# Kernel tuning notes

Hardware: AMD Instinct MI355X
Metric: run time of the kernel (lower is better)

Reference implementation:

```python
import jax, jax.numpy as jnp
import numpy as np

B, T, D = 1, 2048, 1024
H = 16
HD = D // H
K = 4
FF = 4 * D
LAYERS = 24
EPS = 1.1920929e-07  # torch.finfo(float32).eps, RMSNorm default


def setup_inputs() -> dict:
    key = jax.random.key(0)
    ks = jax.random.split(key, 16)
    s = 0.02
    return {
        "x": jax.random.normal(ks[0], (B, T, D), jnp.float32),
        "gamma": jax.random.uniform(ks[1], (D,), jnp.float32),
        "beta": jax.random.normal(ks[2], (D,), jnp.float32) * 0.1,
        "iter_scale": jax.random.uniform(ks[3], (1,), jnp.float32),
        "qkv_bases": jax.random.normal(ks[4], (K, 3 * D, D), jnp.float32) * s,
        "o_bases": jax.random.normal(ks[5], (K, D, D), jnp.float32) * s,
        "gate_bases": jax.random.normal(ks[6], (K, FF, D), jnp.float32) * s,
        "up_bases": jax.random.normal(ks[7], (K, FF, D), jnp.float32) * s,
        "down_bases": jax.random.normal(ks[8], (K, D, FF), jnp.float32) * s,
        "alpha_qkv": jax.random.normal(ks[9], (LAYERS, K), jnp.float32) * 0.1 + jnp.eye(LAYERS, K)[:, :K] * 0.0 + jnp.concatenate([jnp.ones((LAYERS, 1)), jnp.zeros((LAYERS, K - 1))], axis=1),
        "alpha_o": jnp.concatenate([jnp.ones((LAYERS, 1)), jnp.zeros((LAYERS, K - 1))], axis=1) + jax.random.normal(ks[10], (LAYERS, K)) * 0.1,
        "alpha_gate": jnp.concatenate([jnp.ones((LAYERS, 1)), jnp.zeros((LAYERS, K - 1))], axis=1) + jax.random.normal(ks[11], (LAYERS, K)) * 0.1,
        "alpha_up": jnp.concatenate([jnp.ones((LAYERS, 1)), jnp.zeros((LAYERS, K - 1))], axis=1) + jax.random.normal(ks[12], (LAYERS, K)) * 0.1,
        "alpha_down": jnp.concatenate([jnp.ones((LAYERS, 1)), jnp.zeros((LAYERS, K - 1))], axis=1) + jax.random.normal(ks[13], (LAYERS, K)) * 0.1,
        "norm1_w": jnp.ones((D,), jnp.float32),
        "norm2_w": jnp.ones((D,), jnp.float32),
        "layer_idx": 5,
    }


def _rmsnorm(x, w):
    return x * jax.lax.rsqrt(jnp.mean(x * x, axis=-1, keepdims=True) + EPS) * w


def reference(x, gamma, beta, iter_scale, qkv_bases, o_bases, gate_bases, up_bases,
              down_bases, alpha_qkv, alpha_o, alpha_gate, alpha_up, alpha_down,
              norm1_w, norm2_w, layer_idx):
    Bx, Tx, Dx = x.shape
    # --- attention sub-block ---
    h = _rmsnorm(x, norm1_w) * gamma + beta
    W_qkv = jnp.einsum('k,kij->ij', alpha_qkv[layer_idx], qkv_bases)  # [3D, D]
    qkv = jnp.einsum('btd,od->bto', h, W_qkv).reshape(Bx, Tx, 3, H, HD)
    qkv = jnp.transpose(qkv, (2, 0, 3, 1, 4))  # [3, B, H, T, HD]
    q, k, v = qkv[0], qkv[1], qkv[2]
    scores = jnp.einsum('bhqd,bhkd->bhqk', q, k) / jnp.sqrt(jnp.asarray(HD, x.dtype))
    causal = jnp.tril(jnp.ones((Tx, Tx), bool))
    scores = jnp.where(causal, scores, jnp.asarray(-jnp.inf, scores.dtype))
    attn = jax.nn.softmax(scores, axis=-1)
    out = jnp.einsum('bhqk,bhkd->bhqd', attn, v)
    out = jnp.transpose(out, (0, 2, 1, 3)).reshape(Bx, Tx, Dx)
    W_o = jnp.einsum('k,kij->ij', alpha_o[layer_idx], o_bases)
    x_attn = x + jnp.einsum('btd,od->bto', out, W_o)
    # --- SwiGLU FFN sub-block ---
    h2 = _rmsnorm(x_attn, norm2_w) * gamma + beta
    W_g = jnp.einsum('k,kij->ij', alpha_gate[layer_idx], gate_bases)
    W_u = jnp.einsum('k,kij->ij', alpha_up[layer_idx], up_bases)
    W_d = jnp.einsum('k,kij->ij', alpha_down[layer_idx], down_bases)
    gate = jnp.einsum('btd,fd->btf', h2, W_g)
    up = jnp.einsum('btd,fd->btf', h2, W_u)
    ffn_out = jnp.einsum('btf,df->btd', jax.nn.silu(gate) * up, W_d)
    block_out = x_attn + ffn_out
    return x + (block_out - x) * iter_scale
```

## Files before the change

kernel.cpp:

```cpp
#include <hip/hip_runtime.h>
#include <hip/hip_bf16.h>
#include <math.h>

typedef __bf16 bf16;
typedef __bf16 bf16x8 __attribute__((ext_vector_type(8)));
typedef __bf16 bf16x4 __attribute__((ext_vector_type(4)));
typedef float f32x4 __attribute__((ext_vector_type(4)));

#define EPSc 1.1920929e-07f
#define LOG2E 1.44269504f

static __device__ __forceinline__ void glds16(const void* g, void* l) {
  __builtin_amdgcn_global_load_lds((const __attribute__((address_space(1))) void*)g,
                                   (__attribute__((address_space(3))) void*)l, 16, 0, 0);
}

static __device__ __forceinline__ bf16x4 comb4(const float* b0, const float* b1,
                                               const float* b2, const float* b3,
                                               float a0, float a1, float a2, float a3) {
  float4 v0 = *(const float4*)b0, v1 = *(const float4*)b1;
  float4 v2 = *(const float4*)b2, v3 = *(const float4*)b3;
  bf16x4 o;
  o[0] = (bf16)(a0*v0.x + a1*v1.x + a2*v2.x + a3*v3.x);
  o[1] = (bf16)(a0*v0.y + a1*v1.y + a2*v2.y + a3*v3.y);
  o[2] = (bf16)(a0*v0.z + a1*v1.z + a2*v2.z + a3*v3.z);
  o[3] = (bf16)(a0*v0.w + a1*v1.w + a2*v2.w + a3*v3.w);
  return o;
}

__global__ __launch_bounds__(256)
void prep1(const float* __restrict__ qkv_b, const float* __restrict__ a_qkv,
           const float* __restrict__ o_b,   const float* __restrict__ a_o,
           const float* __restrict__ x, const float* __restrict__ n1w,
           const float* __restrict__ gamma, const float* __restrict__ beta,
           const int* __restrict__ lidx,
           bf16* __restrict__ Wqkv, bf16* __restrict__ Wo, bf16* __restrict__ hbuf) {
  const int bid = blockIdx.x, tid = threadIdx.x;
  if (bid < 4096) {
    int li = lidx[0];
    const float* base; const float* al; bf16* out; size_t flat, n;
    if (bid < 3072) { base = qkv_b; al = a_qkv; out = Wqkv; flat = (size_t)bid << 10; n = (size_t)3072*1024; }
    else            { base = o_b;   al = a_o;   out = Wo;   flat = (size_t)(bid-3072) << 10; n = (size_t)1024*1024; }
    float a0 = al[li*4], a1 = al[li*4+1], a2 = al[li*4+2], a3 = al[li*4+3];
    size_t off = flat + tid*4;
    bf16x4 o = comb4(base+off, base+n+off, base+2*n+off, base+3*n+off, a0, a1, a2, a3);
    *(bf16x4*)&out[off] = o;
  } else {
    int row = bid - 4096, t = tid;
    const float4* xr = (const float4*)(x + (size_t)row*1024);
    float4 v = xr[t];
    float ss = v.x*v.x + v.y*v.y + v.z*v.z + v.w*v.w;
    #pragma unroll
    for (int off = 32; off > 0; off >>= 1) ss += __shfl_down(ss, off, 64);
    __shared__ float red[4];
    if ((t & 63) == 0) red[t >> 6] = ss;
    __syncthreads();
    float tot = red[0] + red[1] + red[2] + red[3];
    float r = rsqrtf(tot * (1.0f/1024.0f) + EPSc);
    float4 wv = ((const float4*)n1w)[t];
    float4 gv = ((const float4*)gamma)[t];
    float4 bv = ((const float4*)beta)[t];
    bf16x4 o;
    o[0] = (bf16)(v.x*r*wv.x*gv.x + bv.x);
    o[1] = (bf16)(v.y*r*wv.y*gv.y + bv.y);
    o[2] = (bf16)(v.z*r*wv.z*gv.z + bv.z);
    o[3] = (bf16)(v.w*r*wv.w*gv.w + bv.w);
    *(bf16x4*)&hbuf[(size_t)row*1024 + t*4] = o;
  }
}

__global__ __launch_bounds__(256) void rmsnorm_k(const float* __restrict__ x,
                                                 const float* __restrict__ w,
                                                 const float* __restrict__ gamma,
                                                 const float* __restrict__ beta,
                                                 bf16* __restrict__ out) {
  int row = blockIdx.x, t = threadIdx.x;
  const float4* xr = (const float4*)(x + (size_t)row*1024);
  float4 v = xr[t];
  float ss = v.x*v.x + v.y*v.y + v.z*v.z + v.w*v.w;
  #pragma unroll
  for (int off = 32; off > 0; off >>= 1) ss += __shfl_down(ss, off, 64);
  __shared__ float red[4];
  if ((t & 63) == 0) red[t >> 6] = ss;
  __syncthreads();
  float tot = red[0] + red[1] + red[2] + red[3];
  float r = rsqrtf(tot * (1.0f/1024.0f) + EPSc);
  float4 wv = ((const float4*)w)[t];
  float4 gv = ((const float4*)gamma)[t];
  float4 bv = ((const float4*)beta)[t];
  bf16x4 o;
  o[0] = (bf16)(v.x*r*wv.x*gv.x + bv.x);
  o[1] = (bf16)(v.y*r*wv.y*gv.y + bv.y);
  o[2] = (bf16)(v.z*r*wv.z*gv.z + bv.z);
  o[3] = (bf16)(v.w*r*wv.w*gv.w + bv.w);
  *(bf16x4*)&out[(size_t)row*1024 + t*4] = o;
}

template<int EP, int NTW>
__global__ __launch_bounds__(256)
void gemm_bt(const bf16* __restrict__ A, const bf16* __restrict__ Bw,
             int M, int N, int K, int lda, int ldb, int gx,
             float* __restrict__ outf, bf16* __restrict__ outb,
             const float* __restrict__ auxf, const float* __restrict__ auxf2,
             const float* __restrict__ iscale) {
  constexpr int BN = NTW * 32;
  __shared__ __align__(16) bf16 As[2][128*64];
  __shared__ __align__(16) bf16 Bs[2][BN*64];
  const int nwg = gridDim.x;
  const int orig = blockIdx.x;
  const int wg = (orig & 7) * (nwg >> 3) + (orig >> 3);
  const int tn0 = (wg % gx) * BN, tm0 = (wg / gx) * 128;
  const int tid = threadIdx.x, wave = tid >> 6, lane = tid & 63;
  const int lr = lane & 15, lg = lane >> 4;
  const int wr = wave >> 1, wc = wave & 1;
  f32x4 acc[4][NTW] = {};
  const int rs = lane >> 3;
  const int sc = (((lane & 7) ^ rs) << 3);
  const int x0 = ((lg ^ (lr & 7)) << 3);
  const int x1 = (((4 + lg) ^ (lr & 7)) << 3);

  const bf16* Abase = A + (size_t)tm0 * lda;
  const bf16* Bbase = Bw + (size_t)tn0 * ldb;

  auto stage = [&](bf16* as, bf16* bs, int k0) {
    #pragma unroll
    for (int j = 0; j < 4; ++j) {
      int chunk = wave*4 + j;
      int r = chunk*8 + rs;
      glds16(Abase + (size_t)r*lda + k0 + sc, as + chunk*512 + lane*8);
    }
    #pragma unroll
    for (int j = 0; j < NTW; ++j) {
      int chunk = wave*NTW + j;
      int r = chunk*8 + rs;
      glds16(Bbase + (size_t)r*ldb + k0 + sc, bs + chunk*512 + lane*8);
    }
  };
  auto comp = [&](const bf16* as, const bf16* bs) {
    #pragma unroll
    for (int kk = 0; kk < 2; ++kk) {
      const int x = kk ? x1 : x0;
      bf16x8 av[4], bv[NTW];
      #pragma unroll
      for (int m = 0; m < 4; ++m) av[m] = *(const bf16x8*)&as[(wr*64 + m*16 + lr)*64 + x];
      #pragma unroll
      for (int n = 0; n < NTW; ++n) bv[n] = *(const bf16x8*)&bs[(wc*NTW*16 + n*16 + lr)*64 + x];
      #pragma unroll
      for (int m = 0; m < 4; ++m)
        #pragma unroll
        for (int n = 0; n < NTW; ++n)
          acc[m][n] = __builtin_amdgcn_mfma_f32_16x16x32_bf16(av[m], bv[n], acc[m][n], 0, 0, 0);
    }
  };

  bf16 *a0 = As[0], *a1 = As[1], *b0 = Bs[0], *b1 = Bs[1];
  stage(a0, b0, 0);
  __syncthreads();
  for (int k0 = 64; k0 < K; k0 += 64) {
    stage(a1, b1, k0);
    comp(a0, b0);
    __syncthreads();
    bf16* t;
    t = a0; a0 = a1; a1 = t;
    t = b0; b0 = b1; b1 = t;
  }
  comp(a0, b0);

  float its = 0.f;
  if constexpr (EP == 4) its = iscale[0];
  #pragma unroll
  for (int m = 0; m < 4; ++m)
    #pragma unroll
    for (int n = 0; n < NTW; ++n)
      #pragma unroll
      for (int i = 0; i < 4; ++i) {
        int row = tm0 + wr*64 + m*16 + lg*4 + i;
        int col = tn0 + wc*NTW*16 + n*16 + lr;
        size_t idx = (size_t)row * N + col;
        float v = acc[m][n][i];
        if constexpr (EP == 0) outb[idx] = (bf16)v;
        else if constexpr (EP == 1) outf[idx] = auxf[idx] + v;
        else if constexpr (EP == 4) {
          float xv = auxf[idx], xa = auxf2[idx];
          outf[idx] = xv + (xa + v - xv) * its;
        }
      }
}

__global__ __launch_bounds__(512, 2)
void gemm_gu256(const bf16* __restrict__ A, const bf16* __restrict__ Bw,
                bf16* __restrict__ outb) {
  __shared__ __align__(16) bf16 L[2][2][2][8192];
  const int orig = blockIdx.x;
  const int wg = (orig & 7) * 32 + (orig >> 3);
  const int tn0 = (wg & 31) * 256, tm0 = (wg >> 5) * 256;
  const int tid = threadIdx.x, wave = tid >> 6, lane = tid & 63;
  const int lr = lane & 15, lg = lane >> 4;
  const int wr = wave >> 2, wn = wave & 3;
  const int rs8 = lane >> 3;
  const int gc8 = (((lane & 7) ^ rs8) << 3);
  const int xk0 = ((lg ^ (lr & 7)) << 3);
  const int xk1 = (((4 + lg) ^ (lr & 7)) << 3);
  f32x4 acc[8][4] = {};

  const bf16* Ab = A + (size_t)tm0 * 1024;
  const bf16* Bb = Bw + (size_t)tn0 * 1024;

  auto stage_half = [&](bf16* dst, const bf16* gbase, int half, int k0) {
    #pragma unroll
    for (int l = 0; l < 2; ++l) {
      int r = half*128 + (wave*2 + l)*8 + rs8;
      glds16(gbase + (size_t)r*1024 + k0 + gc8, dst + (wave*2 + l)*512 + lane*8);
    }
  };

  stage_half(&L[0][0][0][0], Ab, 0, 0);
  stage_half(&L[0][0][1][0], Ab, 1, 0);
  stage_half(&L[0][1][0][0], Bb, 0, 0);
  stage_half(&L[0][1][1][0], Bb, 1, 0);
  stage_half(&L[1][1][0][0], Bb, 0, 64);
  stage_half(&L[1][1][1][0], Bb, 1, 64);
  asm volatile("s_waitcnt vmcnt(4)" ::: "memory");
  __builtin_amdgcn_s_barrier();

  for (int t = 0; t < 16; ++t) {
    const int b = t & 1;
    const bf16* ah = &L[b][0][wr][0];
    const bf16* bh = &L[b][1][wn >> 1][0];
    bf16x8 breg[4][2];
    #pragma unroll
    for (int p = 0; p < 4; ++p) {
      if (p == 0) {
        #pragma unroll
        for (int n = 0; n < 4; ++n) {
          int row = (wn & 1)*64 + n*16 + lr;
          breg[n][0] = *(const bf16x8*)&bh[row*64 + xk0];
          breg[n][1] = *(const bf16x8*)&bh[row*64 + xk1];
        }
      }
      bf16x8 av[2][2];
      #pragma unroll
      for (int mi = 0; mi < 2; ++mi) {
        int row = p*32 + mi*16 + lr;
        av[mi][0] = *(const bf16x8*)&ah[row*64 + xk0];
        av[mi][1] = *(const bf16x8*)&ah[row*64 + xk1];
      }
      if (p == 0 && t < 15) stage_half(&L[b^1][0][0][0], Ab, 0, (t+1)*64);
      if (p == 1 && t < 15) stage_half(&L[b^1][0][1][0], Ab, 1, (t+1)*64);
      if (p == 2 && t < 14) stage_half(&L[b][1][0][0], Bb, 0, (t+2)*64);
      if (p == 3 && t < 14) stage_half(&L[b][1][1][0], Bb, 1, (t+2)*64);
      __builtin_amdgcn_s_barrier();
      __builtin_amdgcn_s_setprio(1);
      #pragma unroll
      for (int mi = 0; mi < 2; ++mi)
        #pragma unroll
        for (int n = 0; n < 4; ++n) {
          acc[p*2+mi][n] = __builtin_amdgcn_mfma_f32_16x16x32_bf16(av[mi][0], breg[n][0], acc[p*2+mi][n], 0, 0, 0);
          acc[p*2+mi][n] = __builtin_amdgcn_mfma_f32_16x16x32_bf16(av[mi][1], breg[n][1], acc[p*2+mi][n], 0, 0, 0);
        }
      __builtin_amdgcn_s_setprio(0);
      if (p == 3) {
        if (t >= 14) asm volatile("s_waitcnt vmcnt(0)" ::: "memory");
        else         asm volatile("s_waitcnt vmcnt(4)" ::: "memory");
      }
      __builtin_amdgcn_s_barrier();
    }
  }

  #pragma unroll
  for (int mf = 0; mf < 8; ++mf)
    #pragma unroll
    for (int j = 0; j < 2; ++j)
      #pragma unroll
      for (int i = 0; i < 4; ++i) {
        int row = tm0 + wr*128 + mf*16 + lg*4 + i;
        int col = (tn0 >> 1) + wn*32 + j*16 + lr;
        float g = acc[mf][2*j][i], u = acc[mf][2*j+1][i];
        float s = g / (1.f + __builtin_amdgcn_exp2f(-g * LOG2E));
        outb[(size_t)row * 4096 + col] = (bf16)(s * u);
      }
}

__global__ __launch_bounds__(256)
void attn_mega(const bf16* __restrict__ qkv, bf16* __restrict__ out,
               const float* __restrict__ gate_b, const float* __restrict__ up_b,
               const float* __restrict__ down_b,
               const float* __restrict__ a_gate, const float* __restrict__ a_up,
               const float* __restrict__ a_down, const int* __restrict__ lidx,
               bf16* __restrict__ Wgu, bf16* __restrict__ Wd) {
  __shared__ __align__(16) bf16 Ks[2][64*72];
  __shared__ __align__(16) bf16 Vt[2][64*66];
  __shared__ __align__(16) bf16 Ps[4][16*68];
  const int bid = blockIdx.x;
  const int tid = threadIdx.x;

  if (bid < 256) {
    const int cb = bid;
    int li = lidx[0];
    float g0 = a_gate[li*4], g1 = a_gate[li*4+1], g2 = a_gate[li*4+2], g3 = a_gate[li*4+3];
    float u0 = a_up[li*4],   u1 = a_up[li*4+1],   u2 = a_up[li*4+2],   u3 = a_up[li*4+3];
    float d0 = a_down[li*4], d1 = a_down[li*4+1], d2 = a_down[li*4+2], d3 = a_down[li*4+3];
    const size_t PS = (size_t)4096 * 1024;
    for (int it = 0; it < 48; ++it) {
      int chunk = it * 256 + cb;
      if (chunk < 8192) {
        int r = chunk, w = r & 31;
        int f = ((r >> 5) << 4) + (w & 15);
        const float* base = (w < 16) ? gate_b : up_b;
        float a0 = (w < 16) ? g0 : u0, a1 = (w < 16) ? g1 : u1;
        float a2 = (w < 16) ? g2 : u2, a3 = (w < 16) ? g3 : u3;
        size_t src = (size_t)f*1024 + tid*4;
        bf16x4 o = comb4(base+src, base+PS+src, base+2*PS+src, base+3*PS+src, a0, a1, a2, a3);
        *(bf16x4*)&Wgu[((size_t)r << 10) + tid*4] = o;
      } else {
        size_t off = ((size_t)(chunk - 8192) << 10) + tid*4;
        bf16x4 o = comb4(down_b+off, down_b+PS+off, down_b+2*PS+off, down_b+3*PS+off, d0, d1, d2, d3);
        *(bf16x4*)&Wd[off] = o;
      }
    }
    return;
  }

  const int a = bid - 256;
  const int qb = 31 - (a >> 4);
  const int h = (a & 7) + 8 * ((a >> 3) & 1);
  const int wave = tid >> 6, lane = tid & 63;
  const int lr = lane & 15, lg = lane >> 4;
  const int q0 = qb * 64;

  bf16x8 qf[2];
  {
    const bf16* qrow = qkv + (size_t)(q0 + wave*16 + lr)*3072 + h*64;
    qf[0] = *(const bf16x8*)(qrow + lg*8);
    qf[1] = *(const bf16x8*)(qrow + 32 + lg*8);
  }
  f32x4 o[4] = {};
  float mrow = -__builtin_inff(), lrow = 0.f;
  const int xsrc = (lane & 48) + ((lane >> 4) << 2);

  const int r0 = tid >> 3, r1 = (tid + 256) >> 3;
  const int c0 = (tid & 7) << 3;
  const bf16* kb = qkv + 1024 + h*64 + c0;
  const bf16* vb = qkv + 2048 + h*64 + c0;

  bf16x8 kreg[2], vreg[2];
  auto stage_load = [&](int kv0) {
    kreg[0] = *(const bf16x8*)(kb + (size_t)(kv0 + r0)*3072);
    kreg[1] = *(const bf16x8*)(kb + (size_t)(kv0 + r1)*3072);
    vreg[0] = *(const bf16x8*)(vb + (size_t)(kv0 + r0)*3072);
    vreg[1] = *(const bf16x8*)(vb + (size_t)(kv0 + r1)*3072);
  };
  auto stage_write = [&](int buf) {
    *(bf16x8*)&Ks[buf][r0*72 + c0] = kreg[0];
    *(bf16x8*)&Ks[buf][r1*72 + c0] = kreg[1];
    #pragma unroll
    for (int e = 0; e < 8; ++e) Vt[buf][(c0 + e)*66 + r0] = vreg[0][e];
    #pragma unroll
    for (int e = 0; e < 8; ++e) Vt[buf][(c0 + e)*66 + r1] = vreg[1][e];
  };

  stage_load(0);
  stage_write(0);
  __syncthreads();
  int cur = 0;

  const float C = 0.125f * LOG2E;

  for (int t = 0; t <= qb; ++t) {
    const int kv0 = t * 64;
    if (t < qb) stage_load(kv0 + 64);

    f32x4 s[4] = {};
    __builtin_amdgcn_s_setprio(1);
    #pragma unroll
    for (int n = 0; n < 4; ++n) {
      bf16x8 k0f = *(const bf16x8*)&Ks[cur][(n*16 + lr)*72 + lg*8];
      s[n] = __builtin_amdgcn_mfma_f32_16x16x32_bf16(k0f, qf[0], s[n], 0, 0, 0);
      bf16x8 k1f = *(const bf16x8*)&Ks[cur][(n*16 + lr)*72 + 32 + lg*8];
      s[n] = __builtin_amdgcn_mfma_f32_16x16x32_bf16(k1f, qf[1], s[n], 0, 0, 0);
    }
    __builtin_amdgcn_s_setprio(0);

    if (t == qb) {
      const int qv = q0 + wave*16 + lr;
      #pragma unroll
      for (int n = 0; n < 4; ++n)
        #pragma unroll
        for (int i = 0; i < 4; ++i)
          if (kv0 + n*16 + lg*4 + i > qv) s[n][i] = -__builtin_inff();
    }

    float mnew;
    {
      f32x4 t0 = s[0], t1 = s[1];
      #pragma unroll
      for (int i = 0; i < 4; ++i) { t0[i] = fmaxf(t0[i], s[2][i]); t1[i] = fmaxf(t1[i], s[3][i]); }
      float a0 = fmaxf(t0[0], t0[1]), a1 = fmaxf(t0[2], t0[3]);
      float b0 = fmaxf(t1[0], t1[1]), b1 = fmaxf(t1[2], t1[3]);
      mnew = fmaxf(fmaxf(a0, a1), fmaxf(b0, b1));
    }
    mnew = fmaxf(mnew, __shfl_xor(mnew, 16, 64));
    mnew = fmaxf(mnew, __shfl_xor(mnew, 32, 64));

    float pmn = mnew * C;
    if (__any(pmn > mrow + 8.f)) {
      float mt = fmaxf(mrow, pmn);
      float fc = __builtin_amdgcn_exp2f(mrow - mt);
      mrow = mt;
      lrow *= fc;
      #pragma unroll
      for (int i = 0; i < 4; ++i) {
        float fci = __shfl(fc, xsrc + i, 64);
        #pragma unroll
        for (int nd = 0; nd < 4; ++nd) o[nd][i] *= fci;
      }
    }

    float rsum = 0.f;
    #pragma unroll
    for (int n = 0; n < 4; ++n)
      #pragma unroll
      for (int i = 0; i < 4; ++i) {
        float e = __builtin_amdgcn_exp2f(__builtin_fmaf(s[n][i], C, -mrow));
        s[n][i] = e;
        rsum += e;
      }
    rsum += __shfl_xor(rsum, 16, 64);
    rsum += __shfl_xor(rsum, 32, 64);
    lrow += rsum;

    #pragma unroll
    for (int n = 0; n < 4; ++n) {
      bf16x4 p4;
      #pragma unroll
      for (int i = 0; i < 4; ++i) p4[i] = (bf16)s[n][i];
      *(bf16x4*)&Ps[wave][lr*68 + n*16 + lg*4] = p4;
    }
    asm volatile("s_waitcnt lgkmcnt(0)" ::: "memory");
    __builtin_amdgcn_s_setprio(1);
    #pragma unroll
    for (int kk = 0; kk < 2; ++kk) {
      bf16x8 pf = *(const bf16x8*)&Ps[wave][lr*68 + kk*32 + lg*8];
      #pragma unroll
      for (int nd = 0; nd < 4; ++nd) {
        bf16x8 vf = *(const bf16x8*)&Vt[cur][(nd*16 + lr)*66 + kk*32 + lg*8];
        o[nd] = __builtin_amdgcn_mfma_f32_16x16x32_bf16(pf, vf, o[nd], 0, 0, 0);
      }
    }
    __builtin_amdgcn_s_setprio(0);
    if (t < qb) {
      stage_write(cur ^ 1);
      __syncthreads();
      cur ^= 1;
    }
  }
  #pragma unroll
  for (int i = 0; i < 4; ++i) {
    float li = __shfl(lrow, xsrc + i, 64);
    float inv = 1.f / li;
    #pragma unroll
    for (int nd = 0; nd < 4; ++nd)
      out[(size_t)(q0 + wave*16 + lg*4 + i)*1024 + h*64 + nd*16 + lr] = (bf16)(o[nd][i]*inv);
  }
}

extern "C" void kernel_launch(void* const* d_in, const int* in_sizes, int n_in,
                              void* d_out, int out_size, void* d_ws, size_t ws_size,
                              hipStream_t stream) {
  const float* x        = (const float*)d_in[0];
  const float* gamma    = (const float*)d_in[1];
  const float* beta     = (const float*)d_in[2];
  const float* iscale   = (const float*)d_in[3];
  const float* qkv_b    = (const float*)d_in[4];
  const float* o_b      = (const float*)d_in[5];
  const float* gate_b   = (const float*)d_in[6];
  const float* up_b     = (const float*)d_in[7];
  const float* down_b   = (const float*)d_in[8];
  const float* a_qkv    = (const float*)d_in[9];
  const float* a_o      = (const float*)d_in[10];
  const float* a_gate   = (const float*)d_in[11];
  const float* a_up     = (const float*)d_in[12];
  const float* a_down   = (const float*)d_in[13];
  const float* n1w      = (const float*)d_in[14];
  const float* n2w      = (const float*)d_in[15];
  const int*   lidx     = (const int*)d_in[16];

  char* p = (char*)d_ws;
  auto alloc = [&](size_t bytes) { char* r = p; p += (bytes + 255) & ~(size_t)255; return r; };
  bf16*  Wqkv = (bf16*)alloc((size_t)3072*1024*2);
  bf16*  Wo   = (bf16*)alloc((size_t)1024*1024*2);
  bf16*  Wgu  = (bf16*)alloc((size_t)8192*1024*2);
  bf16*  Wd   = (bf16*)alloc((size_t)1024*4096*2);
  bf16*  hbuf = (bf16*)alloc((size_t)2048*1024*2);
  bf16*  qkvb = (bf16*)alloc((size_t)2048*3072*2);
  bf16*  attn = (bf16*)alloc((size_t)2048*1024*2);
  float* xat  = (float*)alloc((size_t)2048*1024*4);
  bf16*  h2   = (bf16*)alloc((size_t)2048*1024*2);
  bf16*  act  = (bf16*)alloc((size_t)2048*4096*2);
  float* out  = (float*)d_out;

  prep1<<<6144, 256, 0, stream>>>(qkv_b, a_qkv, o_b, a_o, x, n1w, gamma, beta, lidx,
                                  Wqkv, Wo, hbuf);
  gemm_bt<0,4><<<24*16, 256, 0, stream>>>(hbuf, Wqkv, 2048, 3072, 1024, 1024, 1024, 24,
                                          nullptr, qkvb, nullptr, nullptr, nullptr);
  attn_mega<<<768, 256, 0, stream>>>(qkvb, attn, gate_b, up_b, down_b,
                                     a_gate, a_up, a_down, lidx, Wgu, Wd);
  gemm_bt<1,2><<<16*16, 256, 0, stream>>>(attn, Wo, 2048, 1024, 1024, 1024, 1024, 16,
                                          xat, nullptr, x, nullptr, nullptr);
  rmsnorm_k<<<2048, 256, 0, stream>>>(xat, n2w, gamma, beta, h2);
  gemm_gu256<<<256, 512, 0, stream>>>(h2, Wgu, act);
  gemm_bt<4,2><<<16*16, 256, 0, stream>>>(act, Wd, 2048, 1024, 4096, 4096, 4096, 16,
                                          out, nullptr, x, xat, iscale);
}
```

Measured before the change: 193.5 us.

## Enlarge attention query tile to 128 rows with two 16-row tiles per wave

Each attention block now handles 128 query rows (32 per wave, two 16-row sub-tiles) instead of 64, so every K/V tile staged into LDS feeds twice as many MFMAs. This halves the attention block count and the K/V global loads and LDS staging per query, and reuses each K and V fragment across both sub-tiles. In exchange, register pressure rises, there are fewer blocks and the causal workload is coarser, which may hurt load balance. The mask condition is generalised to the per-wave diagonal, and the max reference is clamped to guard against fully masked rows.

```diff
diff --git a/kernel.cpp b/kernel.cpp
--- a/kernel.cpp
+++ b/kernel.cpp
@@ -290,7 +290,7 @@
                bf16* __restrict__ Wgu, bf16* __restrict__ Wd) {
   __shared__ __align__(16) bf16 Ks[2][64*72];
   __shared__ __align__(16) bf16 Vt[2][64*66];
-  __shared__ __align__(16) bf16 Ps[4][16*68];
+  __shared__ __align__(16) bf16 Ps[4][2][16*72];
   const int bid = blockIdx.x;
   const int tid = threadIdx.x;
 
@@ -322,23 +322,27 @@
   }
 
   const int a = bid - 256;
-  const int qb = 31 - (a >> 4);
-  const int h = (a & 7) + 8 * ((a >> 3) & 1);
+  const int qb = 15 - (a >> 4);
+  const int h = a & 15;
   const int wave = tid >> 6, lane = tid & 63;
   const int lr = lane & 15, lg = lane >> 4;
-  const int q0 = qb * 64;
-
-  bf16x8 qf[2];
-  {
-    const bf16* qrow = qkv + (size_t)(q0 + wave*16 + lr)*3072 + h*64;
-    qf[0] = *(const bf16x8*)(qrow + lg*8);
-    qf[1] = *(const bf16x8*)(qrow + 32 + lg*8);
+  const int q0 = qb * 128;
+  const int qw = q0 + wave * 32;
+
+  bf16x8 qf[2][2];
+  #pragma unroll
+  for (int qt = 0; qt < 2; ++qt) {
+    const bf16* qrow = qkv + (size_t)(qw + qt*16 + lr)*3072 + h*64;
+    qf[qt][0] = *(const bf16x8*)(qrow + lg*8);
+    qf[qt][1] = *(const bf16x8*)(qrow + 32 + lg*8);
   }
-  f32x4 o[4] = {};
-  float mrow = -__builtin_inff(), lrow = 0.f;
-  const int xsrc = (lane & 48) + ((lane >> 4) << 2);
-
-  const int r0 = tid >> 3, r1 = (tid + 256) >> 3;
+  f32x4 o[2][4] = {};
+  float mrow[2], lrow[2];
+  mrow[0] = mrow[1] = -__builtin_inff();
+  lrow[0] = lrow[1] = 0.f;
+  const int xsrc = (lane & 48) | (lg << 2);
+
+  const int r0 = tid >> 3, r1 = r0 + 32;
   const int c0 = (tid & 7) << 3;
   const bf16* kb = qkv + 1024 + h*64 + c0;
   const bf16* vb = qkv + 2048 + h*64 + c0;
@@ -365,103 +369,117 @@
   int cur = 0;
 
   const float C = 0.125f * LOG2E;
-
-  for (int t = 0; t <= qb; ++t) {
+  const int nt = 2 * (qb + 1);
+
+  for (int t = 0; t < nt; ++t) {
     const int kv0 = t * 64;
-    if (t < qb) stage_load(kv0 + 64);
-
-    f32x4 s[4] = {};
+    if (t < nt-1) stage_load(kv0 + 64);
+
+    f32x4 s[2][4] = {};
     __builtin_amdgcn_s_setprio(1);
     #pragma unroll
     for (int n = 0; n < 4; ++n) {
       bf16x8 k0f = *(const bf16x8*)&Ks[cur][(n*16 + lr)*72 + lg*8];
-      s[n] = __builtin_amdgcn_mfma_f32_16x16x32_bf16(k0f, qf[0], s[n], 0, 0, 0);
       bf16x8 k1f = *(const bf16x8*)&Ks[cur][(n*16 + lr)*72 + 32 + lg*8];
-      s[n] = __builtin_amdgcn_mfma_f32_16x16x32_bf16(k1f, qf[1], s[n], 0, 0, 0);
+      #pragma unroll
+      for (int qt = 0; qt < 2; ++qt) {
+        s[qt][n] = __builtin_amdgcn_mfma_f32_16x16x32_bf16(k0f, qf[qt][0], s[qt][n], 0, 0, 0);
+        s[qt][n] = __builtin_amdgcn_mfma_f32_16x16x32_bf16(k1f, qf[qt][1], s[qt][n], 0, 0, 0);
+      }
     }
     __builtin_amdgcn_s_setprio(0);
 
-    if (t == qb) {
-      const int qv = q0 + wave*16 + lr;
-      #pragma unroll
-      for (int n = 0; n < 4; ++n)
+    if (kv0 + 63 > qw) {
+      #pragma unroll
+      for (int qt = 0; qt < 2; ++qt) {
+        const int qv = qw + qt*16 + lr;
         #pragma unroll
-        for (int i = 0; i < 4; ++i)
-          if (kv0 + n*16 + lg*4 + i > qv) s[n][i] = -__builtin_inff();
-    }
-
-    float mnew;
-    {
-      f32x4 t0 = s[0], t1 = s[1];
-      #pragma unroll
-      for (int i = 0; i < 4; ++i) { t0[i] = fmaxf(t0[i], s[2][i]); t1[i] = fmaxf(t1[i], s[3][i]); }
+        for (int n = 0; n < 4; ++n)
+          #pragma unroll
+          for (int i = 0; i < 4; ++i)
+            if (kv0 + n*16 + lg*4 + i > qv) s[qt][n][i] = -__builtin_inff();
+      }
+    }
+
+    float pmn[2];
+    #pragma unroll
+    for (int qt = 0; qt < 2; ++qt) {
+      f32x4 t0 = s[qt][0], t1 = s[qt][1];
+      #pragma unroll
+      for (int i = 0; i < 4; ++i) { t0[i] = fmaxf(t0[i], s[qt][2][i]); t1[i] = fmaxf(t1[i], s[qt][3][i]); }
       float a0 = fmaxf(t0[0], t0[1]), a1 = fmaxf(t0[2], t0[3]);
       float b0 = fmaxf(t1[0], t1[1]), b1 = fmaxf(t1[2], t1[3]);
-      mnew = fmaxf(fmaxf(a0, a1), fmaxf(b0, b1));
-    }
-    mnew = fmaxf(mnew, __shfl_xor(mnew, 16, 64));
-    mnew = fmaxf(mnew, __shfl_xor(mnew, 32, 64));
-
-    float pmn = mnew * C;
-    if (__any(pmn > mrow + 8.f)) {
-      float mt = fmaxf(mrow, pmn);
-      float fc = __builtin_amdgcn_exp2f(mrow - mt);
-      mrow = mt;
-      lrow *= fc;
-      #pragma unroll
-      for (int i = 0; i < 4; ++i) {
-        float fci = __shfl(fc, xsrc + i, 64);
+      float mnew = fmaxf(fmaxf(a0, a1), fmaxf(b0, b1));
+      mnew = fmaxf(mnew, __shfl_xor(mnew, 16, 64));
+      mnew = fmaxf(mnew, __shfl_xor(mnew, 32, 64));
+      pmn[qt] = mnew * C;
+    }
+    bool grow = (pmn[0] > mrow[0] + 8.f) || (pmn[1] > mrow[1] + 8.f);
+    if (__any(grow)) {
+      #pragma unroll
+      for (int qt = 0; qt < 2; ++qt) {
+        float mt = fmaxf(mrow[qt], pmn[qt]);
+        float fc = __builtin_amdgcn_exp2f(mrow[qt] - mt);
+        mrow[qt] = mt;
+        lrow[qt] *= fc;
         #pragma unroll
-        for (int nd = 0; nd < 4; ++nd) o[nd][i] *= fci;
-      }
-    }
-
-    float rsum = 0.f;
-    #pragma unroll
-    for (int n = 0; n < 4; ++n)
-      #pragma unroll
-      for (int i = 0; i < 4; ++i) {
-        float e = __builtin_amdgcn_exp2f(__builtin_fmaf(s[n][i], C, -mrow));
-        s[n][i] = e;
-        rsum += e;
-      }
-    rsum += __shfl_xor(rsum, 16, 64);
-    rsum += __shfl_xor(rsum, 32, 64);
-    lrow += rsum;
-
-    #pragma unroll
-    for (int n = 0; n < 4; ++n) {
-      bf16x4 p4;
-      #pragma unroll
-      for (int i = 0; i < 4; ++i) p4[i] = (bf16)s[n][i];
-      *(bf16x4*)&Ps[wave][lr*68 + n*16 + lg*4] = p4;
+        for (int i = 0; i < 4; ++i) {
+          float fci = __shfl(fc, xsrc + i, 64);
+          #pragma unroll
+          for (int nd = 0; nd < 4; ++nd) o[qt][nd][i] *= fci;
+        }
+      }
+    }
+    #pragma unroll
+    for (int qt = 0; qt < 2; ++qt) {
+      float mref = fmaxf(mrow[qt], -3e38f);
+      float rsum = 0.f;
+      #pragma unroll
+      for (int n = 0; n < 4; ++n) {
+        bf16x4 p4;
+        #pragma unroll
+        for (int i = 0; i < 4; ++i) {
+          float e = __builtin_amdgcn_exp2f(__builtin_fmaf(s[qt][n][i], C, -mref));
+          rsum += e;
+          p4[i] = (bf16)e;
+        }
+        *(bf16x4*)&Ps[wave][qt][lr*72 + n*16 + lg*4] = p4;
+      }
+      rsum += __shfl_xor(rsum, 16, 64);
+      rsum += __shfl_xor(rsum, 32, 64);
+      lrow[qt] += rsum;
     }
     asm volatile("s_waitcnt lgkmcnt(0)" ::: "memory");
-    __builtin_amdgcn_s_setprio(1);
+
     #pragma unroll
     for (int kk = 0; kk < 2; ++kk) {
-      bf16x8 pf = *(const bf16x8*)&Ps[wave][lr*68 + kk*32 + lg*8];
+      bf16x8 pf0 = *(const bf16x8*)&Ps[wave][0][lr*72 + kk*32 + lg*8];
+      bf16x8 pf1 = *(const bf16x8*)&Ps[wave][1][lr*72 + kk*32 + lg*8];
+      __builtin_amdgcn_s_setprio(1);
       #pragma unroll
       for (int nd = 0; nd < 4; ++nd) {
         bf16x8 vf = *(const bf16x8*)&Vt[cur][(nd*16 + lr)*66 + kk*32 + lg*8];
-        o[nd] = __builtin_amdgcn_mfma_f32_16x16x32_bf16(pf, vf, o[nd], 0, 0, 0);
-      }
-    }
-    __builtin_amdgcn_s_setprio(0);
-    if (t < qb) {
+        o[0][nd] = __builtin_amdgcn_mfma_f32_16x16x32_bf16(pf0, vf, o[0][nd], 0, 0, 0);
+        o[1][nd] = __builtin_amdgcn_mfma_f32_16x16x32_bf16(pf1, vf, o[1][nd], 0, 0, 0);
+      }
+      __builtin_amdgcn_s_setprio(0);
+    }
+    if (t < nt-1) {
       stage_write(cur ^ 1);
       __syncthreads();
       cur ^= 1;
     }
   }
   #pragma unroll
-  for (int i = 0; i < 4; ++i) {
-    float li = __shfl(lrow, xsrc + i, 64);
-    float inv = 1.f / li;
-    #pragma unroll
-    for (int nd = 0; nd < 4; ++nd)
-      out[(size_t)(q0 + wave*16 + lg*4 + i)*1024 + h*64 + nd*16 + lr] = (bf16)(o[nd][i]*inv);
-  }
+  for (int qt = 0; qt < 2; ++qt)
+    #pragma unroll
+    for (int i = 0; i < 4; ++i) {
+      float li = __shfl(lrow[qt], xsrc + i, 64);
+      float inv = 1.f / li;
+      #pragma unroll
+      for (int nd = 0; nd < 4; ++nd)
+        out[(size_t)(qw + qt*16 + lg*4 + i)*1024 + h*64 + nd*16 + lr] = (bf16)(o[qt][nd][i]*inv);
+    }
 }
 
 extern "C" void kernel_launch(void* const* d_in, const int* in_sizes, int n_in,
@@ -503,7 +521,7 @@
                                   Wqkv, Wo, hbuf);
   gemm_bt<0,4><<<24*16, 256, 0, stream>>>(hbuf, Wqkv, 2048, 3072, 1024, 1024, 1024, 24,
                                           nullptr, qkvb, nullptr, nullptr, nullptr);
-  attn_mega<<<768, 256, 0, stream>>>(qkvb, attn, gate_b, up_b, down_b,
+  attn_mega<<<512, 256, 0, stream>>>(qkvb, attn, gate_b, up_b, down_b,
                                      a_gate, a_up, a_down, lidx, Wgu, Wd);
   gemm_bt<1,2><<<16*16, 256, 0, stream>>>(attn, Wo, 2048, 1024, 1024, 1024, 1024, 16,
                                           xat, nullptr, x, nullptr, nullptr);
```

New measurement: 201.7 us. +4.2%, slower.
